# Kernel tuning notes

Hardware: AMD Instinct MI355X
Metric: run time of the kernel (lower is better)

## Reference

```python
import jax, jax.numpy as jnp
import numpy as np

DEPTH = 30
IN_C, OUT_C, WIDTH = 1, 1, 1
DILATIONS = [i + 1 for i in range(10)]


def setup_inputs() -> dict:
    key = jax.random.key(0)
    ks = jax.random.split(key, 9)
    B, H, W = 4, 512, 512
    # MSDConvBlock weight init std from the source
    std = float(np.sqrt(2.0 / (9.0 * (IN_C + WIDTH * (DEPTH - 1)) + OUT_C)))
    x = jax.random.normal(ks[0], (B, IN_C, H, W), dtype=jnp.float32)
    # Wmsd[i, :i+1] are the 3x3 kernels at depth i: channel 0 acts on x,
    # channel z acts on hiddenstate z-1. Padded rows are unused.
    Wmsd = jax.random.normal(ks[1], (DEPTH, DEPTH, 3, 3), dtype=jnp.float32) * std
    bias = jax.random.normal(ks[2], (DEPTH,), dtype=jnp.float32) * 0.1  # shared per-depth bias
    # final 1x1 conv (zero-init in source; random here so the output is non-trivial)
    convW = jax.random.normal(ks[3], (OUT_C, WIDTH * DEPTH + IN_C, 1, 1), dtype=jnp.float32) * 0.1
    convB = jax.random.normal(ks[4], (OUT_C,), dtype=jnp.float32) * 0.1
    # ScalingBlocks: per-channel affine, identity init
    sin_w = jnp.ones((IN_C,), dtype=jnp.float32)
    sin_b = jnp.zeros((IN_C,), dtype=jnp.float32)
    sout_w = jnp.ones((OUT_C,), dtype=jnp.float32)
    sout_b = jnp.zeros((OUT_C,), dtype=jnp.float32)
    return {"x": x, "Wmsd": Wmsd, "bias": bias, "convW": convW, "convB": convB,
            "sin_w": sin_w, "sin_b": sin_b, "sout_w": sout_w, "sout_b": sout_b}


def _conv(x, w, dilation):
    # 'same' 3x3 dilated conv, NCHW / OIHW
    d = dilation
    return jax.lax.conv_general_dilated(
        x, w, window_strides=(1, 1), padding=[(d, d), (d, d)],
        rhs_dilation=(d, d), dimension_numbers=("NCHW", "OIHW", "NCHW"))


def reference(x, Wmsd, bias, convW, convB, sin_w, sin_b, sout_w, sout_b):
    depth = Wmsd.shape[0]
    x = x * sin_w[None, :, None, None] + sin_b[None, :, None, None]
    feats = x  # growing concat: [x, h0, h1, ...]
    for i in range(depth):
        d = DILATIONS[i % len(DILATIONS)]  # counter increments once per depth
        n_in = feats.shape[1]  # = IN_C + i (with width=1, IN_C=1)
        w = Wmsd[i, :n_in][None]  # [1, n_in, 3, 3]
        # sum of single-channel convs == one multi-channel conv over the concat
        h = _conv(feats, w, d)
        h = jax.nn.relu(h + bias[i])
        feats = jnp.concatenate([feats, h], axis=1)
    y = jax.lax.conv_general_dilated(
        feats, convW, window_strides=(1, 1), padding="VALID",
        dimension_numbers=("NCHW", "OIHW", "NCHW"))
    y = y + convB[None, :, None, None]
    y = y * sout_w[None, :, None, None] + sout_b[None, :, None, None]
    return y
```

## Files before the change

kernel.cpp:

```cpp
#include <hip/hip_runtime.h>


#define MSD_DEPTH 30
#define NB 4
#define IH 512
#define IW 512
#define HALO 16
#define WPp (IW + 2 * HALO)
#define HPp (IH + 2 * HALO)
#define PLANE_U ((size_t)WPp * HPp)
#define PSTR ((size_t)NB * PLANE_U)
#define NPAIR 15
#define NPIX (NB * IH * IW)
#define WPK_OFF ((size_t)20 << 20)

typedef _Float16 h2v __attribute__((ext_vector_type(2)));
typedef unsigned int u32;

__device__ __forceinline__ float fdot2u(u32 a, u32 b, float c) {
#if __has_builtin(__builtin_amdgcn_fdot2)
    return __builtin_amdgcn_fdot2(__builtin_bit_cast(h2v, a),
                                  __builtin_bit_cast(h2v, b), c, false);
#else
    h2v x = __builtin_bit_cast(h2v, a), y = __builtin_bit_cast(h2v, b);
    return c + (float)x[0] * (float)y[0] + (float)x[1] * (float)y[1];
#endif
}

__global__ __launch_bounds__(256) void pack_weights(const float* __restrict__ Wmsd,
                                                    const float* __restrict__ convW,
                                                    u32* __restrict__ wpk,
                                                    u32* __restrict__ cpk) {
    int idx = blockIdx.x * 256 + threadIdx.x;
    if (idx < MSD_DEPTH * NPAIR * 9) {
        int I = idx / (NPAIR * 9);
        int rem = idx - I * (NPAIR * 9);
        int p = rem / 9, t = rem - p * 9;
        int NC = I + 1, c0 = 2 * p, c1 = 2 * p + 1;
        h2v pk;
        pk[0] = (_Float16)((c0 < NC) ? Wmsd[((size_t)I * MSD_DEPTH + c0) * 9 + t] : 0.f);
        pk[1] = (_Float16)((c1 < NC) ? Wmsd[((size_t)I * MSD_DEPTH + c1) * 9 + t] : 0.f);
        wpk[idx] = __builtin_bit_cast(u32, pk);
    }
    if (idx < NPAIR) {
        h2v pk;
        pk[0] = (_Float16)convW[2 * idx];
        pk[1] = (_Float16)convW[2 * idx + 1];
        cpk[idx] = __builtin_bit_cast(u32, pk);
    }
}

__global__ __launch_bounds__(256) void zero_halo_kernel(u32* __restrict__ feats) {
    const int per = 32 * (WPp / 4);
    int idx = blockIdx.x * 256 + threadIdx.x;
    if (idx >= per * NPAIR * NB) return;
    int sub = idx / per;
    int s = idx - sub * per;
    int rr = s / 136;
    int c4 = (s - rr * 136) * 4;
    int r = (rr < 16) ? rr : (IH + HALO) + (rr - 16);
    uint4 z = {0, 0, 0, 0};
    *(uint4*)(feats + (size_t)sub * PLANE_U + (size_t)r * WPp + c4) = z;
}

__global__ __launch_bounds__(256) void scale_in_kernel(const float* __restrict__ x,
                                                       u32* __restrict__ feats,
                                                       const float* __restrict__ sw,
                                                       const float* __restrict__ sb) {
    int s = blockIdx.x * 256 + threadIdx.x;
    int idx = s * 8;
    int b = idx >> 18;
    int y = (idx >> 9) & 511;
    int xx = idx & 511;
    const float sws = sw[0], sbs = sb[0];
    u32 v[8];
#pragma unroll
    for (int j = 0; j < 8; ++j) {
        _Float16 h = (_Float16)(x[idx + j] * sws + sbs);
        v[j] = (u32)__builtin_bit_cast(unsigned short, h);
    }
    u32* q = feats + (size_t)b * PLANE_U + (size_t)(y + HALO) * WPp + HALO + xx;
    *(uint4*)q = *(uint4*)&v[0];
    *(uint4*)(q + 4) = *(uint4*)&v[4];
}

template <int I>
__global__ __launch_bounds__(128, 2) void depth_kernel(u32* __restrict__ feats,
                                                       const u32* __restrict__ wpk,
                                                       const u32* __restrict__ cpk,
                                                       const float* __restrict__ bias,
                                                       const float* __restrict__ convW,
                                                       const float* __restrict__ convB,
                                                       const float* __restrict__ soutw,
                                                       const float* __restrict__ soutb,
                                                       float* __restrict__ out) {
    constexpr int D = (I % 10) + 1;
    constexpr int NC = I + 1;
    constexpr int NP = (NC + 1) / 2;
    constexpr bool LAST = (I == MSD_DEPTH - 1);

    const int tid = threadIdx.x;
    const int widx = tid >> 6, lane = tid & 63;
    const int bid = blockIdx.x;
    const int xcd = bid & 7;
    const int kk = bid >> 3;
    const int b = xcd >> 1;
    const int y = (xcd & 1) * 256 + kk * 2 + widx;

    const int bp_m2 = ((lane - 2) & 63) << 2;
    const int bp_m1 = ((lane - 1) & 63) << 2;
    const int bp_p1 = ((lane + 1) & 63) << 2;
    const int bp_p2 = ((lane + 2) & 63) << 2;

    u32* const pb = feats + (size_t)b * PLANE_U + (size_t)(y + HALO) * WPp + HALO + lane * 8;

    float acc[8], ydot[8];
#pragma unroll
    for (int j = 0; j < 8; ++j) { acc[j] = 0.f; ydot[j] = 0.f; }

    const u32* const wrb = wpk + (size_t)I * (NPAIR * 9);

    u32 A[3][8], B[3][8];

    auto load_pair = [&](u32 (*buf)[8], int p) {
        const u32* pp = pb + (size_t)p * PSTR;
#pragma unroll
        for (int r = 0; r < 3; ++r) {
            const u32* rp = pp + (ptrdiff_t)(r - 1) * (D * WPp);
            *(uint4*)&buf[r][0] = *(const uint4*)rp;
            *(uint4*)&buf[r][4] = *(const uint4*)(rp + 4);
        }
    };

    auto window = [&](const u32* d, int shift, u32* w) {
#pragma unroll
        for (int k = 0; k < 8; ++k) {
            int off = k + shift;
            if (off >= 0 && off < 8) {
                w[k] = d[off];
            } else {
                int q = off >> 3;
                int idx = off - q * 8;
                int addr = (q == -2) ? bp_m2
                         : (q == -1) ? bp_m1
                         : (q == 1)  ? bp_p1 : bp_p2;
                u32 t = (u32)__builtin_amdgcn_ds_bpermute(addr, (int)d[idx]);
                bool valid = (q < 0) ? (lane >= -q) : (lane <= 63 - q);
                w[k] = valid ? t : 0u;
            }
        }
    };

    auto compute = [&](u32 (*buf)[8], int p) {
        const u32* wq = wrb + p * 9;
        const u32 cw = LAST ? cpk[p] : 0u;
#pragma unroll
        for (int r = 0; r < 3; ++r) {
            u32* d = buf[r];
            u32 wl[8], wrr[8];
            window(d, -D, wl);
            window(d, D, wrr);
            const u32 w0 = wq[r * 3 + 0], w1 = wq[r * 3 + 1], w2 = wq[r * 3 + 2];
#pragma unroll
            for (int k = 0; k < 8; ++k) {
                float a = acc[k];
                a = fdot2u(wl[k], w0, a);
                a = fdot2u(d[k], w1, a);
                a = fdot2u(wrr[k], w2, a);
                acc[k] = a;
            }
            if (LAST && r == 1) {
#pragma unroll
                for (int k = 0; k < 8; ++k) ydot[k] = fdot2u(d[k], cw, ydot[k]);
            }
        }
    };

    load_pair(A, 0);
    int p = 0;
    for (; p + 2 <= NP; p += 2) {
        load_pair(B, p + 1);
        compute(A, p);
        if (p + 2 < NP) load_pair(A, p + 2);
        compute(B, p + 1);
    }
    if (p < NP) compute(A, p);

    const float b0 = bias[I];
    if (!LAST) {
        u32 part[8];
        if constexpr ((NC & 1) != 0) {
            const u32* rp = pb + (size_t)(NP - 1) * PSTR;
            *(uint4*)&part[0] = *(const uint4*)rp;
            *(uint4*)&part[4] = *(const uint4*)(rp + 4);
        }
        u32 mg[8];
#pragma unroll
        for (int j = 0; j < 8; ++j) {
            float h = acc[j] + b0;
            h = h > 0.f ? h : 0.f;
            u32 h16 = (u32)__builtin_bit_cast(unsigned short, (_Float16)h);
            if constexpr ((NC & 1) != 0)
                mg[j] = (part[j] & 0xFFFFu) | (h16 << 16);
            else
                mg[j] = h16;
        }
        u32* q = feats + (size_t)(NC >> 1) * PSTR + (size_t)b * PLANE_U +
                 (size_t)(y + HALO) * WPp + HALO + lane * 8;
        *(uint4*)q = *(uint4*)&mg[0];
        *(uint4*)(q + 4) = *(uint4*)&mg[4];
    } else {
        const float cw30 = convW[MSD_DEPTH];
        const float cb = convB[0], ow = soutw[0], ob = soutb[0];
        float* q = out + ((size_t)b * IH + y) * IW + lane * 8;
        float o[8];
#pragma unroll
        for (int j = 0; j < 8; ++j) {
            float h = acc[j] + b0;
            h = h > 0.f ? h : 0.f;
            float yv = ydot[j] + cw30 * h + cb;
            o[j] = yv * ow + ob;
        }
        *(uint4*)q = *(uint4*)&o[0];
        *(uint4*)(q + 4) = *(uint4*)&o[4];
    }
}

extern "C" void kernel_launch(void* const* d_in, const int* in_sizes, int n_in,
                              void* d_out, int out_size, void* d_ws, size_t ws_size,
                              hipStream_t stream) {
    const float* x     = (const float*)d_in[0];
    const float* Wmsd  = (const float*)d_in[1];
    const float* bias  = (const float*)d_in[2];
    const float* convW = (const float*)d_in[3];
    const float* convB = (const float*)d_in[4];
    const float* sinw  = (const float*)d_in[5];
    const float* sinb  = (const float*)d_in[6];
    const float* soutw = (const float*)d_in[7];
    const float* soutb = (const float*)d_in[8];
    float* out = (float*)d_out;

    u32* feats = (u32*)d_ws;
    u32* wpk = feats + WPK_OFF;
    u32* cpk = wpk + MSD_DEPTH * NPAIR * 9;

    pack_weights<<<16, 256, 0, stream>>>(Wmsd, convW, wpk, cpk);

    const int zstrips = 32 * (WPp / 4) * NPAIR * NB;
    zero_halo_kernel<<<(zstrips + 255) / 256, 256, 0, stream>>>(feats);

    scale_in_kernel<<<NPIX / 8 / 256, 256, 0, stream>>>(x, feats, sinw, sinb);

#define LNCH(I) depth_kernel<I><<<1024, 128, 0, stream>>>(feats, wpk, cpk, bias, convW, convB, soutw, soutb, out);
    LNCH(0)  LNCH(1)  LNCH(2)  LNCH(3)  LNCH(4)
    LNCH(5)  LNCH(6)  LNCH(7)  LNCH(8)  LNCH(9)
    LNCH(10) LNCH(11) LNCH(12) LNCH(13) LNCH(14)
    LNCH(15) LNCH(16) LNCH(17) LNCH(18) LNCH(19)
    LNCH(20) LNCH(21) LNCH(22) LNCH(23) LNCH(24)
    LNCH(25) LNCH(26) LNCH(27) LNCH(28) LNCH(29)
#undef LNCH
}
```

Measured before the change: 395.3 us.

## Split channel-pair loop across two waves per row with LDS reduction

Each block now handles one image row instead of two. The two wavefronts split the channel-pair range in half and merge their partial accumulators through shared memory, with the first wave writing the output. The grid doubles to 2048 blocks and the launch bound asks for 4 blocks per CU. This aims to expose more parallelism and shorten each wave's serial chain, at the cost of a barrier, LDS traffic and an idle second wave during the epilogue.

```diff
diff --git a/kernel.cpp b/kernel.cpp
--- a/kernel.cpp
+++ b/kernel.cpp
@@ -85,7 +85,7 @@
 }
 
 template <int I>
-__global__ __launch_bounds__(128, 2) void depth_kernel(u32* __restrict__ feats,
+__global__ __launch_bounds__(128, 4) void depth_kernel(u32* __restrict__ feats,
                                                        const u32* __restrict__ wpk,
                                                        const u32* __restrict__ cpk,
                                                        const float* __restrict__ bias,
@@ -97,15 +97,19 @@
     constexpr int D = (I % 10) + 1;
     constexpr int NC = I + 1;
     constexpr int NP = (NC + 1) / 2;
+    constexpr int NPh = (NP + 1) / 2;
     constexpr bool LAST = (I == MSD_DEPTH - 1);
 
+    __shared__ float redacc[8][64];
+    __shared__ float redyd[LAST ? 8 : 1][64];
+
     const int tid = threadIdx.x;
-    const int widx = tid >> 6, lane = tid & 63;
+    const int w = tid >> 6, lane = tid & 63;
     const int bid = blockIdx.x;
     const int xcd = bid & 7;
     const int kk = bid >> 3;
     const int b = xcd >> 1;
-    const int y = (xcd & 1) * 256 + kk * 2 + widx;
+    const int y = (xcd & 1) * 256 + kk;
 
     const int bp_m2 = ((lane - 2) & 63) << 2;
     const int bp_m1 = ((lane - 1) & 63) << 2;
@@ -132,12 +136,12 @@
         }
     };
 
-    auto window = [&](const u32* d, int shift, u32* w) {
+    auto window = [&](const u32* d, int shift, u32* wd) {
 #pragma unroll
         for (int k = 0; k < 8; ++k) {
             int off = k + shift;
             if (off >= 0 && off < 8) {
-                w[k] = d[off];
+                wd[k] = d[off];
             } else {
                 int q = off >> 3;
                 int idx = off - q * 8;
@@ -146,7 +150,7 @@
                          : (q == 1)  ? bp_p1 : bp_p2;
                 u32 t = (u32)__builtin_amdgcn_ds_bpermute(addr, (int)d[idx]);
                 bool valid = (q < 0) ? (lane >= -q) : (lane <= 63 - q);
-                w[k] = valid ? t : 0u;
+                wd[k] = valid ? t : 0u;
             }
         }
     };
@@ -176,15 +180,36 @@
         }
     };
 
-    load_pair(A, 0);
-    int p = 0;
-    for (; p + 2 <= NP; p += 2) {
-        load_pair(B, p + 1);
-        compute(A, p);
-        if (p + 2 < NP) load_pair(A, p + 2);
-        compute(B, p + 1);
-    }
-    if (p < NP) compute(A, p);
+    const int p0 = w ? NPh : 0;
+    const int p1 = w ? NP : NPh;
+    if (p1 > p0) {
+        load_pair(A, p0);
+        int p = p0;
+        for (; p + 2 <= p1; p += 2) {
+            load_pair(B, p + 1);
+            compute(A, p);
+            if (p + 2 < p1) load_pair(A, p + 2);
+            compute(B, p + 1);
+        }
+        if (p < p1) compute(A, p);
+    }
+
+    if (w == 1) {
+#pragma unroll
+        for (int j = 0; j < 8; ++j) redacc[j][lane] = acc[j];
+        if constexpr (LAST) {
+#pragma unroll
+            for (int j = 0; j < 8; ++j) redyd[j][lane] = ydot[j];
+        }
+    }
+    __syncthreads();
+    if (w != 0) return;
+#pragma unroll
+    for (int j = 0; j < 8; ++j) acc[j] += redacc[j][lane];
+    if constexpr (LAST) {
+#pragma unroll
+        for (int j = 0; j < 8; ++j) ydot[j] += redyd[j][lane];
+    }
 
     const float b0 = bias[I];
     if (!LAST) {
@@ -251,7 +276,7 @@
 
     scale_in_kernel<<<NPIX / 8 / 256, 256, 0, stream>>>(x, feats, sinw, sinb);
 
-#define LNCH(I) depth_kernel<I><<<1024, 128, 0, stream>>>(feats, wpk, cpk, bias, convW, convB, soutw, soutb, out);
+#define LNCH(I) depth_kernel<I><<<2048, 128, 0, stream>>>(feats, wpk, cpk, bias, convW, convB, soutw, soutb, out);
     LNCH(0)  LNCH(1)  LNCH(2)  LNCH(3)  LNCH(4)
     LNCH(5)  LNCH(6)  LNCH(7)  LNCH(8)  LNCH(9)
     LNCH(10) LNCH(11) LNCH(12) LNCH(13) LNCH(14)
```

Result: slower. 593.1 us (+50.0%).

## Assign rows to blocks by dilation stride so waves share halo rows

Applied to the files above, without the earlier changes.

Each block now has four waves, and they handle rows y, y+D, y+2D and y+3D in the same residue class modulo the dilation, rather than two adjacent rows. The aim is for the rows each wave loads at y±D to overlap with the rows its neighbouring waves compute, which should improve L2/cache reuse of the input channels. The grid size is now computed per dilation, with early exit for out-of-range rows, and the block size doubles to 256 threads. The risk is some idle waves in the tail blocks and a different XCD-to-data mapping.

```diff
diff --git a/kernel.cpp b/kernel.cpp
--- a/kernel.cpp
+++ b/kernel.cpp
@@ -85,7 +85,7 @@
 }
 
 template <int I>
-__global__ __launch_bounds__(128, 2) void depth_kernel(u32* __restrict__ feats,
+__global__ __launch_bounds__(256, 2) void depth_kernel(u32* __restrict__ feats,
                                                        const u32* __restrict__ wpk,
                                                        const u32* __restrict__ cpk,
                                                        const float* __restrict__ bias,
@@ -98,14 +98,22 @@
     constexpr int NC = I + 1;
     constexpr int NP = (NC + 1) / 2;
     constexpr bool LAST = (I == MSD_DEPTH - 1);
+    constexpr int L = (IH + D - 1) / D;
+    constexpr int K = (L + 3) / 4;
+    constexpr int KH = (K + 1) / 2;
 
     const int tid = threadIdx.x;
-    const int widx = tid >> 6, lane = tid & 63;
+    const int w = tid >> 6, lane = tid & 63;
     const int bid = blockIdx.x;
     const int xcd = bid & 7;
-    const int kk = bid >> 3;
+    const int j = bid >> 3;
     const int b = xcd >> 1;
-    const int y = (xcd & 1) * 256 + kk * 2 + widx;
+    const int half = xcd & 1;
+    const int kk = j / D;
+    const int r = j - kk * D;
+    const int k = half * KH + kk;
+    const int y = r + (4 * k + w) * D;
+    if (k >= K || y >= IH) return;
 
     const int bp_m2 = ((lane - 2) & 63) << 2;
     const int bp_m1 = ((lane - 1) & 63) << 2;
@@ -116,7 +124,7 @@
 
     float acc[8], ydot[8];
 #pragma unroll
-    for (int j = 0; j < 8; ++j) { acc[j] = 0.f; ydot[j] = 0.f; }
+    for (int q = 0; q < 8; ++q) { acc[q] = 0.f; ydot[q] = 0.f; }
 
     const u32* const wrb = wpk + (size_t)I * (NPAIR * 9);
 
@@ -125,19 +133,19 @@
     auto load_pair = [&](u32 (*buf)[8], int p) {
         const u32* pp = pb + (size_t)p * PSTR;
 #pragma unroll
-        for (int r = 0; r < 3; ++r) {
-            const u32* rp = pp + (ptrdiff_t)(r - 1) * (D * WPp);
-            *(uint4*)&buf[r][0] = *(const uint4*)rp;
-            *(uint4*)&buf[r][4] = *(const uint4*)(rp + 4);
+        for (int rr = 0; rr < 3; ++rr) {
+            const u32* rp = pp + (ptrdiff_t)(rr - 1) * (D * WPp);
+            *(uint4*)&buf[rr][0] = *(const uint4*)rp;
+            *(uint4*)&buf[rr][4] = *(const uint4*)(rp + 4);
         }
     };
 
-    auto window = [&](const u32* d, int shift, u32* w) {
-#pragma unroll
-        for (int k = 0; k < 8; ++k) {
-            int off = k + shift;
+    auto window = [&](const u32* d, int shift, u32* wd) {
+#pragma unroll
+        for (int kq = 0; kq < 8; ++kq) {
+            int off = kq + shift;
             if (off >= 0 && off < 8) {
-                w[k] = d[off];
+                wd[kq] = d[off];
             } else {
                 int q = off >> 3;
                 int idx = off - q * 8;
@@ -146,7 +154,7 @@
                          : (q == 1)  ? bp_p1 : bp_p2;
                 u32 t = (u32)__builtin_amdgcn_ds_bpermute(addr, (int)d[idx]);
                 bool valid = (q < 0) ? (lane >= -q) : (lane <= 63 - q);
-                w[k] = valid ? t : 0u;
+                wd[kq] = valid ? t : 0u;
             }
         }
     };
@@ -155,23 +163,23 @@
         const u32* wq = wrb + p * 9;
         const u32 cw = LAST ? cpk[p] : 0u;
 #pragma unroll
-        for (int r = 0; r < 3; ++r) {
-            u32* d = buf[r];
+        for (int rr = 0; rr < 3; ++rr) {
+            u32* d = buf[rr];
             u32 wl[8], wrr[8];
             window(d, -D, wl);
             window(d, D, wrr);
-            const u32 w0 = wq[r * 3 + 0], w1 = wq[r * 3 + 1], w2 = wq[r * 3 + 2];
-#pragma unroll
-            for (int k = 0; k < 8; ++k) {
-                float a = acc[k];
-                a = fdot2u(wl[k], w0, a);
-                a = fdot2u(d[k], w1, a);
-                a = fdot2u(wrr[k], w2, a);
-                acc[k] = a;
+            const u32 w0 = wq[rr * 3 + 0], w1 = wq[rr * 3 + 1], w2 = wq[rr * 3 + 2];
+#pragma unroll
+            for (int kq = 0; kq < 8; ++kq) {
+                float a = acc[kq];
+                a = fdot2u(wl[kq], w0, a);
+                a = fdot2u(d[kq], w1, a);
+                a = fdot2u(wrr[kq], w2, a);
+                acc[kq] = a;
             }
-            if (LAST && r == 1) {
-#pragma unroll
-                for (int k = 0; k < 8; ++k) ydot[k] = fdot2u(d[k], cw, ydot[k]);
+            if (LAST && rr == 1) {
+#pragma unroll
+                for (int kq = 0; kq < 8; ++kq) ydot[kq] = fdot2u(d[kq], cw, ydot[kq]);
             }
         }
     };
@@ -196,34 +204,42 @@
         }
         u32 mg[8];
 #pragma unroll
-        for (int j = 0; j < 8; ++j) {
-            float h = acc[j] + b0;
+        for (int q = 0; q < 8; ++q) {
+            float h = acc[q] + b0;
             h = h > 0.f ? h : 0.f;
             u32 h16 = (u32)__builtin_bit_cast(unsigned short, (_Float16)h);
             if constexpr ((NC & 1) != 0)
-                mg[j] = (part[j] & 0xFFFFu) | (h16 << 16);
+                mg[q] = (part[q] & 0xFFFFu) | (h16 << 16);
             else
-                mg[j] = h16;
-        }
-        u32* q = feats + (size_t)(NC >> 1) * PSTR + (size_t)b * PLANE_U +
-                 (size_t)(y + HALO) * WPp + HALO + lane * 8;
-        *(uint4*)q = *(uint4*)&mg[0];
-        *(uint4*)(q + 4) = *(uint4*)&mg[4];
+                mg[q] = h16;
+        }
+        u32* q2 = feats + (size_t)(NC >> 1) * PSTR + (size_t)b * PLANE_U +
+                  (size_t)(y + HALO) * WPp + HALO + lane * 8;
+        *(uint4*)q2 = *(uint4*)&mg[0];
+        *(uint4*)(q2 + 4) = *(uint4*)&mg[4];
     } else {
         const float cw30 = convW[MSD_DEPTH];
         const float cb = convB[0], ow = soutw[0], ob = soutb[0];
-        float* q = out + ((size_t)b * IH + y) * IW + lane * 8;
+        float* q2 = out + ((size_t)b * IH + y) * IW + lane * 8;
         float o[8];
 #pragma unroll
-        for (int j = 0; j < 8; ++j) {
-            float h = acc[j] + b0;
+        for (int q = 0; q < 8; ++q) {
+            float h = acc[q] + b0;
             h = h > 0.f ? h : 0.f;
-            float yv = ydot[j] + cw30 * h + cb;
-            o[j] = yv * ow + ob;
-        }
-        *(uint4*)q = *(uint4*)&o[0];
-        *(uint4*)(q + 4) = *(uint4*)&o[4];
-    }
+            float yv = ydot[q] + cw30 * h + cb;
+            o[q] = yv * ow + ob;
+        }
+        *(uint4*)q2 = *(uint4*)&o[0];
+        *(uint4*)(q2 + 4) = *(uint4*)&o[4];
+    }
+}
+
+static inline int nblk(int I) {
+    int D = (I % 10) + 1;
+    int L = (IH + D - 1) / D;
+    int K = (L + 3) / 4;
+    int KH = (K + 1) / 2;
+    return 8 * D * KH;
 }
 
 extern "C" void kernel_launch(void* const* d_in, const int* in_sizes, int n_in,
@@ -251,7 +267,7 @@
 
     scale_in_kernel<<<NPIX / 8 / 256, 256, 0, stream>>>(x, feats, sinw, sinb);
 
-#define LNCH(I) depth_kernel<I><<<1024, 128, 0, stream>>>(feats, wpk, cpk, bias, convW, convB, soutw, soutb, out);
+#define LNCH(I) depth_kernel<I><<<nblk(I), 256, 0, stream>>>(feats, wpk, cpk, bias, convW, convB, soutw, soutb, out);
     LNCH(0)  LNCH(1)  LNCH(2)  LNCH(3)  LNCH(4)
     LNCH(5)  LNCH(6)  LNCH(7)  LNCH(8)  LNCH(9)
     LNCH(10) LNCH(11) LNCH(12) LNCH(13) LNCH(14)
```

Result: slower. 454.4 us (+15.0%).
